# Kernel optimization log

Hardware: AMD Instinct MI355X
Metric: run time of the kernel (lower is better)

The kernel has to match this reference:

```python
import jax, jax.numpy as jnp
import numpy as np

EPS = float(jnp.finfo(jnp.float32).eps)


def _mlp(x, W1, b1, W2, b2, W3, b3):
    h = jax.nn.relu(x @ W1 + b1)
    h = jax.nn.relu(h @ W2 + b2)
    return h @ W3 + b3


def setup_inputs() -> dict:
    B, D_A, D_B, K, H = 131072, 16, 16, 32, 256
    key = jax.random.key(0)
    ks = jax.random.split(key, 13)
    def lin(k, fi, fo):
        return jax.random.normal(k, (fi, fo), jnp.float32) * (fi ** -0.5)
    inp = {
        "x": jax.random.uniform(ks[0], (B, D_A + D_B), jnp.float32),
        "hW1": lin(ks[1], D_A, H), "hb1": jnp.zeros((H,), jnp.float32),
        "hW2": lin(ks[2], H, H),   "hb2": jnp.zeros((H,), jnp.float32),
        "hW3": lin(ks[3], H, D_B * (K + 1)), "hb3": jnp.zeros((D_B * (K + 1),), jnp.float32),
        "wW1": lin(ks[4], D_A, H), "wb1": jnp.zeros((H,), jnp.float32),
        "wW2": lin(ks[5], H, H),   "wb2": jnp.zeros((H,), jnp.float32),
        "wW3": lin(ks[6], H, D_B * K), "wb3": jnp.zeros((D_B * K,), jnp.float32),
        "A_dims": jnp.arange(0, 32, 2, dtype=jnp.int32),
        "B_dims": jnp.arange(1, 32, 2, dtype=jnp.int32),
    }
    return inp


def reference(x, hW1, hb1, hW2, hb2, hW3, hb3, wW1, wb1, wW2, wb2, wW3, wb3, A_dims, B_dims):
    B = x.shape[0]
    D_B = B_dims.shape[0]
    K = wW3.shape[1] // D_B
    x_A = x[:, A_dims]               # (B, D_A)
    x_B = x[:, B_dims]               # (B, D_B)

    raw_h = _mlp(x_A, hW1, hb1, hW2, hb2, hW3, hb3).reshape(B, D_B, K + 1)
    heights = jax.nn.softplus(raw_h) + EPS
    raw_w = _mlp(x_A, wW1, wb1, wW2, wb2, wW3, wb3).reshape(B, D_B, K)
    widths = jax.nn.softmax(raw_w, axis=-1)
    zeros = jnp.zeros((B, D_B, 1), x.dtype)
    bins = jnp.concatenate([zeros, jnp.cumsum(widths, axis=-1)], axis=-1)  # (B, D_B, K+1)

    # preprocess_params_2: normalise PDF heights and bin areas
    bin_widths = bins[:, :, 1:] - bins[:, :, :-1]
    bin_areas = 0.5 * (heights[:, :, :-1] + heights[:, :, 1:]) * bin_widths  # (B, D_B, K)
    total_area = bin_areas.sum(axis=-1, keepdims=True)
    v = heights / total_area
    bin_areas = bin_areas / total_area

    # bin search
    i = jnp.sum(x_B[..., None] >= bins, axis=-1) - 1
    i = jnp.clip(i, 0, K - 1)                                  # (B, D_B)
    iu = i[..., None]

    x_left = jnp.take_along_axis(bins, iu, axis=2)[..., 0]
    x_right = jnp.take_along_axis(bins, iu + 1, axis=2)[..., 0]
    w_b = x_right - x_left
    v_left = jnp.take_along_axis(v, iu, axis=2)[..., 0]
    v_right = jnp.take_along_axis(v, iu + 1, axis=2)[..., 0]
    w_v = v_right - v_left

    alpha = (x_B - x_left) / (w_b + EPS)
    # cumulative area up to left edge of bin i: exclusive prefix sum then gather
    c_edges = jnp.concatenate([zeros, jnp.cumsum(bin_areas, axis=-1)], axis=-1)
    c_left = jnp.take_along_axis(c_edges, iu, axis=2)[..., 0]

    y_B = c_left + 0.5 * alpha ** 2 * w_v * w_b + alpha * v_left * w_b
    y = x.at[:, B_dims].set(y_B)
    return y
```

## Files before the change

kernel.cpp:

```cpp
#include <hip/hip_runtime.h>
#include <cmath>

typedef short short8 __attribute__((ext_vector_type(8)));
typedef float f32x16 __attribute__((ext_vector_type(16)));

#define EPSF 1.1920929e-07f

#define LDS_XA 0
#define LDS_X1 1536
#define LDS_X2 18432
#define LDS_X3 35328
#define LDS_TOTAL 52224

#define OFF1H 0
#define OFF1W 4096
#define OFF2H 8192
#define OFF2W 73728
#define OFF3W 139264
#define OFF3H 270336
#define OFFH32 401408
#define OFFB_BYTES 819200

__device__ __forceinline__ unsigned short f2bf(float f) {
  union { float f; unsigned u; } v; v.f = f;
  return (unsigned short)((v.u + 0x8000u) >> 16);
}
__device__ __forceinline__ float sp_eps(float v) {
  return fmaxf(v, 0.f) + __logf(1.f + __expf(-fabsf(v))) + EPSF;
}
__device__ __forceinline__ int chanm(int m) {
  return (((m >> 2) & 1) << 4) + (m & 3) + ((m >> 3) << 2);
}
__device__ __forceinline__ unsigned cvtpk(float lo, float hi) {
  unsigned r;
  asm("v_cvt_pk_bf16_f32 %0, %1, %2" : "=v"(r) : "v"(lo), "v"(hi));
  return r;
}

__global__ void pack_weights(const float* __restrict__ hW1, const float* __restrict__ wW1,
                             const float* __restrict__ hW2, const float* __restrict__ wW2,
                             const float* __restrict__ hW3, const float* __restrict__ wW3,
                             const float* __restrict__ hb3,
                             unsigned short* __restrict__ out) {
  int bid = blockIdx.x, l = threadIdx.x;
  if (bid == 800) {
    float* fb = (float*)((char*)out + OFFB_BYTES);
    for (int idx = l; idx < 528; idx += 64) {
      int d = idx / 33, j = idx - d * 33;
      if (j < 32) fb[d * 32 + j] = hb3[idx];
      else fb[512 + d] = hb3[idx];
    }
    return;
  }
  int m = l & 31;
  const float* W; unsigned short* dst; int tile, col, NC;
  if (bid < 8)        { W = hW1; dst = out + OFF1H;  tile = bid;       col = tile * 32 + chanm(m); NC = 256; }
  else if (bid < 16)  { W = wW1; dst = out + OFF1W;  tile = bid - 8;   col = tile * 32 + chanm(m); NC = 256; }
  else if (bid < 144) { W = hW2; dst = out + OFF2H;  tile = bid - 16;  col = (tile >> 4) * 32 + chanm(m); NC = 256; }
  else if (bid < 272) { W = wW2; dst = out + OFF2W;  tile = bid - 144; col = (tile >> 4) * 32 + chanm(m); NC = 256; }
  else if (bid < 528) { W = wW3; dst = out + OFF3W;  tile = bid - 272; col = (tile >> 4) * 32 + chanm(m); NC = 512; }
  else if (bid < 784) { W = hW3; dst = out + OFF3H;  tile = bid - 528; col = (tile >> 4) * 33 + chanm(m); NC = 528; }
  else {
    W = hW3; dst = out + OFFH32; tile = bid - 784;
    int qq = (m >> 2) & 1, rr = (m & 3) + ((m >> 3) << 2);
    col = qq ? -1 : rr * 33 + 32; NC = 528;
  }
  int kt = (bid < 16) ? 0 : (tile & 15);
  int K  = (bid < 16) ? 16 : 256;
  int k0 = kt * 16 + (l >> 5) * 8;
  short8 v;
  #pragma unroll
  for (int e = 0; e < 8; e++) {
    float f = (col >= 0 && (k0 + e) < K) ? W[(k0 + e) * NC + col] : 0.f;
    v[e] = (short)f2bf(f);
  }
  *(short8*)(dst + (tile * 64 + l) * 8) = v;
}

__device__ __forceinline__ f32x16 bias_init(const float* __restrict__ b) {
  const float4* bp = (const float4*)b;
  float4 b0 = bp[0], b1 = bp[1], b2 = bp[2], b3 = bp[3];
  f32x16 a;
  a[0] = b0.x;  a[1] = b0.y;  a[2] = b0.z;  a[3] = b0.w;
  a[4] = b1.x;  a[5] = b1.y;  a[6] = b1.z;  a[7] = b1.w;
  a[8] = b2.x;  a[9] = b2.y;  a[10] = b2.z; a[11] = b2.w;
  a[12] = b3.x; a[13] = b3.y; a[14] = b3.z; a[15] = b3.w;
  return a;
}

__device__ __forceinline__ void store_act16(unsigned short* dst, f32x16 a) {
  unsigned pk0 = cvtpk(fmaxf(a[0], 0.f),  fmaxf(a[1], 0.f));
  unsigned pk1 = cvtpk(fmaxf(a[2], 0.f),  fmaxf(a[3], 0.f));
  unsigned pk2 = cvtpk(fmaxf(a[4], 0.f),  fmaxf(a[5], 0.f));
  unsigned pk3 = cvtpk(fmaxf(a[6], 0.f),  fmaxf(a[7], 0.f));
  unsigned pk4 = cvtpk(fmaxf(a[8], 0.f),  fmaxf(a[9], 0.f));
  unsigned pk5 = cvtpk(fmaxf(a[10], 0.f), fmaxf(a[11], 0.f));
  unsigned pk6 = cvtpk(fmaxf(a[12], 0.f), fmaxf(a[13], 0.f));
  unsigned pk7 = cvtpk(fmaxf(a[14], 0.f), fmaxf(a[15], 0.f));
  uint4 p0 = {pk0, pk1, pk2, pk3}, p1 = {pk4, pk5, pk6, pk7};
  *(uint4*)dst = p0;
  *(uint4*)(dst + 8) = p1;
}

__device__ __forceinline__ void l2_phase(const unsigned short* __restrict__ src,
                                         unsigned short* __restrict__ dst,
                                         const unsigned short* __restrict__ aBase,
                                         const float* __restrict__ bias,
                                         int w, int l, int q, int r32) {
  f32x16 acc = bias_init(bias + w * 32 + q * 16);
  const unsigned short* aB = aBase + w * 16 * 512 + l * 8;
  const unsigned short* bB = src + r32 * 264 + q * 8;
  #pragma unroll
  for (int kt = 0; kt < 16; kt++)
    acc = __builtin_amdgcn_mfma_f32_32x32x16_bf16(*(const short8*)(aB + kt * 512),
                                                  *(const short8*)(bB + kt * 16), acc, 0, 0, 0);
  store_act16(dst + r32 * 264 + w * 32 + q * 16, acc);
}

__device__ __forceinline__ void spline_store(f32x16 e, f32x16 hh, int d, int r32, int q,
                                             const float* __restrict__ H32p,
                                             const float* __restrict__ x,
                                             float* __restrict__ y, int r0) {
  int grow = r0 + r32;
  float se = 0.f;
  #pragma unroll
  for (int k = 0; k < 16; k++) se += e[k];
  float so = __shfl_xor(se, 32);
  float s = se + so;
  float h16o = __shfl_xor(hh[0], 32);
  float hlast = q ? H32p[r32 * 16 + d] : h16o;
  float xbv = x[grow * 32 + 2 * d + 1];
  float xbs = xbv * s;
  float bl0 = q ? so : 0.f;
  int fnd = (xbs >= bl0) ? 1 : 0;
  float bl = bl0, cl2 = 0.f, sxl = bl0, sew = e[0], shl = hh[0], shr = hh[1], scl2 = 0.f;
  #pragma unroll
  for (int k = 0; k < 16; k++) {
    float hk = hh[k];
    float hn = (k < 15) ? hh[k + 1] : hlast;
    bool c = (xbs >= bl);
    sxl  = c ? bl   : sxl;
    sew  = c ? e[k] : sew;
    shl  = c ? hk   : shl;
    shr  = c ? hn   : shr;
    scl2 = c ? cl2  : scl2;
    cl2 += (hk + hn) * e[k];
    bl  += e[k];
  }
  float cl2o = __shfl_xor(cl2, 32);
  float S2 = cl2 + cl2o;
  scl2 += q ? cl2o : 0.f;
  int   o_fnd  = __shfl_xor(fnd, 32);
  float o_sxl  = __shfl_xor(sxl, 32);
  float o_sew  = __shfl_xor(sew, 32);
  float o_shl  = __shfl_xor(shl, 32);
  float o_shr  = __shfl_xor(shr, 32);
  float o_scl2 = __shfl_xor(scl2, 32);
  bool other = q ? (fnd == 0) : (o_fnd != 0);
  float gsxl  = other ? o_sxl  : sxl;
  float gsew  = other ? o_sew  : sew;
  float gshl  = other ? o_shl  : shl;
  float gshr  = other ? o_shr  : shr;
  float gscl2 = other ? o_scl2 : scl2;
  float alpha = (xbs - gsxl) / (gsew + EPSF);
  float yv = (gscl2 + (alpha * alpha * (gshr - gshl) + 2.f * alpha * gshl) * gsew) / S2;
  if (q == 0) y[grow * 32 + 2 * d + 1] = yv;
}

__global__ __launch_bounds__(512, 3) void fused_kernel(
    const float* __restrict__ x,
    const float* __restrict__ hb1, const float* __restrict__ hb2,
    const float* __restrict__ wb1, const float* __restrict__ wb2,
    const float* __restrict__ wb3,
    const unsigned short* __restrict__ pw,
    float* __restrict__ y) {
  extern __shared__ char lds[];
  const int t = threadIdx.x;
  const int w = t >> 6, l = t & 63, q = l >> 5, r32 = l & 31;
  const int r0 = blockIdx.x * 32;

  unsigned short* XA = (unsigned short*)(lds + LDS_XA);
  unsigned short* X1 = (unsigned short*)(lds + LDS_X1);
  unsigned short* X2 = (unsigned short*)(lds + LDS_X2);
  unsigned short* X3 = (unsigned short*)(lds + LDS_X3);
  const float* pwf = (const float*)((const char*)pw + OFFB_BYTES);

  if (t < 256) {
    int row = t >> 3, c4 = t & 7;
    float4 v = *(const float4*)(x + (r0 + row) * 32 + c4 * 4);
    y[(r0 + row) * 32 + c4 * 4] = v.x;
    y[(r0 + row) * 32 + c4 * 4 + 2] = v.z;
    unsigned short* xa = XA + row * 24 + c4 * 2;
    xa[0] = f2bf(v.x); xa[1] = f2bf(v.z);
  }
  __syncthreads();

  {
    short8 bx = *(const short8*)(XA + r32 * 24 + q * 8);
    f32x16 ah = bias_init(hb1 + w * 32 + q * 16);
    ah = __builtin_amdgcn_mfma_f32_32x32x16_bf16(
        *(const short8*)(pw + OFF1H + w * 512 + l * 8), bx, ah, 0, 0, 0);
    store_act16(X1 + r32 * 264 + w * 32 + q * 16, ah);
    f32x16 aw = bias_init(wb1 + w * 32 + q * 16);
    aw = __builtin_amdgcn_mfma_f32_32x32x16_bf16(
        *(const short8*)(pw + OFF1W + w * 512 + l * 8), bx, aw, 0, 0, 0);
    store_act16(X2 + r32 * 264 + w * 32 + q * 16, aw);
  }
  __syncthreads();

  l2_phase(X1, X3, pw + OFF2H, hb2, w, l, q, r32);
  __syncthreads();

  f32x16 a32;
  if (w == 0) {
    #pragma unroll
    for (int rr = 0; rr < 16; rr++) a32[rr] = 0.f;
    const unsigned short* a32p = pw + OFFH32 + l * 8;
    const unsigned short* bH = X3 + r32 * 264 + q * 8;
    #pragma unroll
    for (int kt = 0; kt < 16; kt++)
      a32 = __builtin_amdgcn_mfma_f32_32x32x16_bf16(*(const short8*)(a32p + kt * 512),
                                                    *(const short8*)(bH + kt * 16), a32, 0, 0, 0);
  }
  l2_phase(X2, X1, pw + OFF2W, wb2, w, l, q, r32);
  __syncthreads();

  if (w == 0 && q == 0) {
    float* o = (float*)(lds + LDS_X2) + r32 * 16;
    const float* hb32 = pwf + 512;
    #pragma unroll
    for (int g = 0; g < 4; g++) {
      float4 v;
      v.x = sp_eps(a32[4 * g + 0] + hb32[4 * g + 0]);
      v.y = sp_eps(a32[4 * g + 1] + hb32[4 * g + 1]);
      v.z = sp_eps(a32[4 * g + 2] + hb32[4 * g + 2]);
      v.w = sp_eps(a32[4 * g + 3] + hb32[4 * g + 3]);
      *(float4*)(o + 4 * g) = v;
    }
  }

  const float* H32p = (const float*)(lds + LDS_X2);
  #pragma unroll 1
  for (int p = 0; p < 2; p++) {
    const int d = p * 8 + w;
    f32x16 e = bias_init(wb3 + d * 32 + q * 16);
    {
      const unsigned short* aW = pw + OFF3W + d * 16 * 512 + l * 8;
      const unsigned short* bW = X1 + r32 * 264 + q * 8;
      #pragma unroll
      for (int kt = 0; kt < 16; kt++)
        e = __builtin_amdgcn_mfma_f32_32x32x16_bf16(*(const short8*)(aW + kt * 512),
                                                    *(const short8*)(bW + kt * 16), e, 0, 0, 0);
    }
    #pragma unroll
    for (int rr = 0; rr < 16; rr++) e[rr] = __expf(e[rr]);
    f32x16 hh = bias_init(pwf + d * 32 + q * 16);
    {
      const unsigned short* aH = pw + OFF3H + d * 16 * 512 + l * 8;
      const unsigned short* bH = X3 + r32 * 264 + q * 8;
      #pragma unroll
      for (int kt = 0; kt < 16; kt++)
        hh = __builtin_amdgcn_mfma_f32_32x32x16_bf16(*(const short8*)(aH + kt * 512),
                                                     *(const short8*)(bH + kt * 16), hh, 0, 0, 0);
    }
    #pragma unroll
    for (int rr = 0; rr < 16; rr++) hh[rr] = sp_eps(hh[rr]);
    if (p == 0) __syncthreads();
    spline_store(e, hh, d, r32, q, H32p, x, y, r0);
  }
}

extern "C" void kernel_launch(void* const* d_in, const int* in_sizes, int n_in,
                              void* d_out, int out_size, void* d_ws, size_t ws_size,
                              hipStream_t stream) {
  const float* x   = (const float*)d_in[0];
  const float* hW1 = (const float*)d_in[1];
  const float* hb1 = (const float*)d_in[2];
  const float* hW2 = (const float*)d_in[3];
  const float* hb2 = (const float*)d_in[4];
  const float* hW3 = (const float*)d_in[5];
  const float* hb3 = (const float*)d_in[6];
  const float* wW1 = (const float*)d_in[7];
  const float* wb1 = (const float*)d_in[8];
  const float* wW2 = (const float*)d_in[9];
  const float* wb2 = (const float*)d_in[10];
  const float* wW3 = (const float*)d_in[11];
  const float* wb3 = (const float*)d_in[12];
  unsigned short* pw = (unsigned short*)d_ws;

  pack_weights<<<801, 64, 0, stream>>>(hW1, wW1, hW2, wW2, hW3, wW3, hb3, pw);

  hipFuncSetAttribute((const void*)fused_kernel,
                      hipFuncAttributeMaxDynamicSharedMemorySize, LDS_TOTAL);
  fused_kernel<<<4096, 512, LDS_TOTAL, stream>>>(
      x, hb1, hb2, wb1, wb2, wb3, pw, (float*)d_out);
}
```

Baseline: 200.9 us.

## Process 64 rows per block with 16 waves, each wave reusing weight fragments across row tiles

Blocks grow from 32 rows and 8 waves to 64 rows and 16 waves. Layer-1 work is split by network (h or w) across waves, and layer-3 gives each wave one output dimension d, looping over two 32-row tiles so the same weight stream serves twice as many rows. Separate LDS buffers for every activation raise LDS use to about 134 KB. The layer-2 and layer-3 weight loads are amortised over more rows, at the cost of one block per CU and less latency hiding.

```diff
diff --git a/kernel.cpp b/kernel.cpp
--- a/kernel.cpp
+++ b/kernel.cpp
@@ -6,11 +6,13 @@
 
 #define EPSF 1.1920929e-07f
 
-#define LDS_XA 0
-#define LDS_X1 1536
-#define LDS_X2 18432
-#define LDS_X3 35328
-#define LDS_TOTAL 52224
+#define LDS_XA   0
+#define LDS_A1H  2048
+#define LDS_A1W  35840
+#define LDS_A2H  69632
+#define LDS_A2W  103424
+#define LDS_H32  2048
+#define LDS_TOTAL 137216
 
 #define OFF1H 0
 #define OFF1W 4096
@@ -102,33 +104,20 @@
   *(uint4*)(dst + 8) = p1;
 }
 
-__device__ __forceinline__ void l2_phase(const unsigned short* __restrict__ src,
-                                         unsigned short* __restrict__ dst,
-                                         const unsigned short* __restrict__ aBase,
-                                         const float* __restrict__ bias,
-                                         int w, int l, int q, int r32) {
-  f32x16 acc = bias_init(bias + w * 32 + q * 16);
-  const unsigned short* aB = aBase + w * 16 * 512 + l * 8;
-  const unsigned short* bB = src + r32 * 264 + q * 8;
-  #pragma unroll
-  for (int kt = 0; kt < 16; kt++)
-    acc = __builtin_amdgcn_mfma_f32_32x32x16_bf16(*(const short8*)(aB + kt * 512),
-                                                  *(const short8*)(bB + kt * 16), acc, 0, 0, 0);
-  store_act16(dst + r32 * 264 + w * 32 + q * 16, acc);
-}
-
-__device__ __forceinline__ void spline_store(f32x16 e, f32x16 hh, int d, int r32, int q,
+#define MFMA(A, B, C) __builtin_amdgcn_mfma_f32_32x32x16_bf16((A), (B), (C), 0, 0, 0)
+
+__device__ __forceinline__ void spline_store(f32x16 e, f32x16 hh, int d, int rowl, int q,
                                              const float* __restrict__ H32p,
                                              const float* __restrict__ x,
                                              float* __restrict__ y, int r0) {
-  int grow = r0 + r32;
+  int grow = r0 + rowl;
   float se = 0.f;
   #pragma unroll
   for (int k = 0; k < 16; k++) se += e[k];
   float so = __shfl_xor(se, 32);
   float s = se + so;
   float h16o = __shfl_xor(hh[0], 32);
-  float hlast = q ? H32p[r32 * 16 + d] : h16o;
+  float hlast = q ? H32p[rowl * 16 + d] : h16o;
   float xbv = x[grow * 32 + 2 * d + 1];
   float xbs = xbv * s;
   float bl0 = q ? so : 0.f;
@@ -167,7 +156,7 @@
   if (q == 0) y[grow * 32 + 2 * d + 1] = yv;
 }
 
-__global__ __launch_bounds__(512, 3) void fused_kernel(
+__global__ __launch_bounds__(1024, 1) void fused_kernel(
     const float* __restrict__ x,
     const float* __restrict__ hb1, const float* __restrict__ hb2,
     const float* __restrict__ wb1, const float* __restrict__ wb2,
@@ -177,56 +166,76 @@
   extern __shared__ char lds[];
   const int t = threadIdx.x;
   const int w = t >> 6, l = t & 63, q = l >> 5, r32 = l & 31;
-  const int r0 = blockIdx.x * 32;
-
-  unsigned short* XA = (unsigned short*)(lds + LDS_XA);
-  unsigned short* X1 = (unsigned short*)(lds + LDS_X1);
-  unsigned short* X2 = (unsigned short*)(lds + LDS_X2);
-  unsigned short* X3 = (unsigned short*)(lds + LDS_X3);
+  const int r0 = blockIdx.x * 64;
+
+  unsigned short* XA  = (unsigned short*)(lds + LDS_XA);
+  unsigned short* A1H = (unsigned short*)(lds + LDS_A1H);
+  unsigned short* A1W = (unsigned short*)(lds + LDS_A1W);
+  unsigned short* A2H = (unsigned short*)(lds + LDS_A2H);
+  unsigned short* A2W = (unsigned short*)(lds + LDS_A2W);
   const float* pwf = (const float*)((const char*)pw + OFFB_BYTES);
 
-  if (t < 256) {
+  if (t < 512) {
     int row = t >> 3, c4 = t & 7;
     float4 v = *(const float4*)(x + (r0 + row) * 32 + c4 * 4);
     y[(r0 + row) * 32 + c4 * 4] = v.x;
     y[(r0 + row) * 32 + c4 * 4 + 2] = v.z;
-    unsigned short* xa = XA + row * 24 + c4 * 2;
+    unsigned short* xa = XA + row * 16 + c4 * 2;
     xa[0] = f2bf(v.x); xa[1] = f2bf(v.z);
   }
   __syncthreads();
 
+  const bool netH = (w >= 8);
+  const int ct = w & 7;
+
   {
-    short8 bx = *(const short8*)(XA + r32 * 24 + q * 8);
-    f32x16 ah = bias_init(hb1 + w * 32 + q * 16);
-    ah = __builtin_amdgcn_mfma_f32_32x32x16_bf16(
-        *(const short8*)(pw + OFF1H + w * 512 + l * 8), bx, ah, 0, 0, 0);
-    store_act16(X1 + r32 * 264 + w * 32 + q * 16, ah);
-    f32x16 aw = bias_init(wb1 + w * 32 + q * 16);
-    aw = __builtin_amdgcn_mfma_f32_32x32x16_bf16(
-        *(const short8*)(pw + OFF1W + w * 512 + l * 8), bx, aw, 0, 0, 0);
-    store_act16(X2 + r32 * 264 + w * 32 + q * 16, aw);
+    const float* b1 = netH ? hb1 : wb1;
+    unsigned short* A1n = netH ? A1H : A1W;
+    short8 af = *(const short8*)(pw + (netH ? OFF1H : OFF1W) + (ct * 64 + l) * 8);
+    #pragma unroll
+    for (int rt = 0; rt < 2; rt++) {
+      short8 bx = *(const short8*)(XA + (rt * 32 + r32) * 16 + q * 8);
+      f32x16 acc = bias_init(b1 + ct * 32 + q * 16);
+      acc = MFMA(af, bx, acc);
+      store_act16(A1n + (rt * 32 + r32) * 264 + ct * 32 + q * 16, acc);
+    }
   }
   __syncthreads();
 
-  l2_phase(X1, X3, pw + OFF2H, hb2, w, l, q, r32);
+  const int p2ct = w & 7, p2rt = w >> 3;
+  {
+    f32x16 acc = bias_init(hb2 + p2ct * 32 + q * 16);
+    const unsigned short* aB = pw + OFF2H + (p2ct * 16 * 64 + l) * 8;
+    const unsigned short* bB = A1H + (p2rt * 32 + r32) * 264 + q * 8;
+    #pragma unroll
+    for (int kt = 0; kt < 16; kt++)
+      acc = MFMA(*(const short8*)(aB + kt * 512), *(const short8*)(bB + kt * 16), acc);
+    store_act16(A2H + (p2rt * 32 + r32) * 264 + p2ct * 32 + q * 16, acc);
+  }
   __syncthreads();
 
   f32x16 a32;
-  if (w == 0) {
+  const bool do32 = (w < 2);
+  if (do32) {
     #pragma unroll
     for (int rr = 0; rr < 16; rr++) a32[rr] = 0.f;
     const unsigned short* a32p = pw + OFFH32 + l * 8;
-    const unsigned short* bH = X3 + r32 * 264 + q * 8;
-    #pragma unroll
-    for (int kt = 0; kt < 16; kt++)
-      a32 = __builtin_amdgcn_mfma_f32_32x32x16_bf16(*(const short8*)(a32p + kt * 512),
-                                                    *(const short8*)(bH + kt * 16), a32, 0, 0, 0);
-  }
-  l2_phase(X2, X1, pw + OFF2W, wb2, w, l, q, r32);
-  __syncthreads();
-
-  if (w == 0 && q == 0) {
-    float* o = (float*)(lds + LDS_X2) + r32 * 16;
+    const unsigned short* bH = A2H + (w * 32 + r32) * 264 + q * 8;
+    #pragma unroll
+    for (int kt = 0; kt < 16; kt++)
+      a32 = MFMA(*(const short8*)(a32p + kt * 512), *(const short8*)(bH + kt * 16), a32);
+  }
+  {
+    f32x16 acc = bias_init(wb2 + p2ct * 32 + q * 16);
+    const unsigned short* aB = pw + OFF2W + (p2ct * 16 * 64 + l) * 8;
+    const unsigned short* bB = A1W + (p2rt * 32 + r32) * 264 + q * 8;
+    #pragma unroll
+    for (int kt = 0; kt < 16; kt++)
+      acc = MFMA(*(const short8*)(aB + kt * 512), *(const short8*)(bB + kt * 16), acc);
+    store_act16(A2W + (p2rt * 32 + r32) * 264 + p2ct * 32 + q * 16, acc);
+  }
+  if (do32 && q == 0) {
+    float* o = (float*)(lds + LDS_H32) + (w * 32 + r32) * 16;
     const float* hb32 = pwf + 512;
     #pragma unroll
     for (int g = 0; g < 4; g++) {
@@ -238,35 +247,33 @@
       *(float4*)(o + 4 * g) = v;
     }
   }
-
-  const float* H32p = (const float*)(lds + LDS_X2);
+  __syncthreads();
+
+  const int d = w;
+  const float* H32p = (const float*)(lds + LDS_H32);
+  const unsigned short* bWt = pw + OFF3W + (d * 16 * 64 + l) * 8;
+  const unsigned short* bHt = pw + OFF3H + (d * 16 * 64 + l) * 8;
+
   #pragma unroll 1
-  for (int p = 0; p < 2; p++) {
-    const int d = p * 8 + w;
+  for (int rt = 0; rt < 2; rt++) {
+    const unsigned short* baw = A2W + (rt * 32 + r32) * 264 + q * 8;
+    const unsigned short* bah = A2H + (rt * 32 + r32) * 264 + q * 8;
+
     f32x16 e = bias_init(wb3 + d * 32 + q * 16);
-    {
-      const unsigned short* aW = pw + OFF3W + d * 16 * 512 + l * 8;
-      const unsigned short* bW = X1 + r32 * 264 + q * 8;
-      #pragma unroll
-      for (int kt = 0; kt < 16; kt++)
-        e = __builtin_amdgcn_mfma_f32_32x32x16_bf16(*(const short8*)(aW + kt * 512),
-                                                    *(const short8*)(bW + kt * 16), e, 0, 0, 0);
-    }
+    #pragma unroll
+    for (int kt = 0; kt < 16; kt++)
+      e = MFMA(*(const short8*)(bWt + kt * 512), *(const short8*)(baw + kt * 16), e);
     #pragma unroll
     for (int rr = 0; rr < 16; rr++) e[rr] = __expf(e[rr]);
+
     f32x16 hh = bias_init(pwf + d * 32 + q * 16);
-    {
-      const unsigned short* aH = pw + OFF3H + d * 16 * 512 + l * 8;
-      const unsigned short* bH = X3 + r32 * 264 + q * 8;
-      #pragma unroll
-      for (int kt = 0; kt < 16; kt++)
-        hh = __builtin_amdgcn_mfma_f32_32x32x16_bf16(*(const short8*)(aH + kt * 512),
-                                                     *(const short8*)(bH + kt * 16), hh, 0, 0, 0);
-    }
+    #pragma unroll
+    for (int kt = 0; kt < 16; kt++)
+      hh = MFMA(*(const short8*)(bHt + kt * 512), *(const short8*)(bah + kt * 16), hh);
     #pragma unroll
     for (int rr = 0; rr < 16; rr++) hh[rr] = sp_eps(hh[rr]);
-    if (p == 0) __syncthreads();
-    spline_store(e, hh, d, r32, q, H32p, x, y, r0);
+
+    spline_store(e, hh, d, rt * 32 + r32, q, H32p, x, y, r0);
   }
 }
 
@@ -292,6 +299,6 @@
 
   hipFuncSetAttribute((const void*)fused_kernel,
                       hipFuncAttributeMaxDynamicSharedMemorySize, LDS_TOTAL);
-  fused_kernel<<<4096, 512, LDS_TOTAL, stream>>>(
+  fused_kernel<<<2048, 1024, LDS_TOTAL, stream>>>(
       x, hb1, hb2, wb1, wb2, wb3, pw, (float*)d_out);
 }
```

After: 716.9 us. 257% more time.
